# Optimization experiments

Measured on AMD Instinct MI355X. Metric: run time of the kernel, lower is better.

Reference implementation:

```python
import jax, jax.numpy as jnp
import numpy as np

N_CLASSES = 1000
N_CONCEPTS = 8
D = 512
BATCH = 4096


def setup_inputs() -> dict:
    key = jax.random.key(0)
    k1, k2 = jax.random.split(key)
    image_encodings = jax.random.normal(k1, (BATCH, D), dtype=jnp.float32)
    description_encodings = jax.random.normal(k2, (N_CLASSES, N_CONCEPTS, D), dtype=jnp.float32)
    return {"image_encodings": image_encodings, "description_encodings": description_encodings}


def reference(image_encodings, description_encodings):
    B, d = image_encodings.shape
    C, K, _ = description_encodings.shape
    # F.normalize(image_encodings, dim=-1)
    img = image_encodings / jnp.linalg.norm(image_encodings, axis=-1, keepdims=True)
    # per-class dot products, stacked over classes and flattened -> [B, C*K]
    sims = jnp.einsum("bd,ckd->bck", img, description_encodings).reshape(B, C * K)
    # descending top-K over all concept similarities (method='rank')
    _, topk_idx = jax.lax.top_k(sims, K)            # [B, K]
    concept_of_class = topk_idx // K                # class bucket of each top concept
    # log-scale rank weights: log1p(ranks)/sum, ranks = K..1
    ranks = jnp.arange(K, 0, -1, dtype=sims.dtype)
    w = jnp.log1p(ranks)
    w = w / jnp.sum(w)
    # weighted vote per class (vectorized scatter-add replaces the per-item dict loop)
    votes = jnp.zeros((B, C), dtype=sims.dtype)
    votes = votes.at[jnp.arange(B)[:, None], concept_of_class].add(w[None, :])
    # dict max over sorted unique keys == argmax with first-index tie-break
    predictions = jnp.argmax(votes, axis=1)
    confidences = jnp.take_along_axis(votes, predictions[:, None], axis=1)[:, 0]
    return predictions.astype(jnp.float32), confidences, sims
```

## Files before the change

kernel.cpp:

```cpp
#include <hip/hip_runtime.h>
#include <math.h>

#define BATCH 4096
#define D 512
#define NCLASS 1000
#define NCON 8
#define NTOT 8000
#define NPAD 8192
#define KH 1024

typedef __attribute__((ext_vector_type(8))) short bf16x8;
typedef __attribute__((ext_vector_type(4))) float f32x4;

static __device__ __forceinline__ unsigned short f2bf(float f) {
    unsigned int u = __float_as_uint(f);
    unsigned int r = (u + 0x7fffu + ((u >> 16) & 1u)) >> 16;
    return (unsigned short)r;
}
static __device__ __forceinline__ float bf2f(unsigned short h) {
    return __uint_as_float(((unsigned int)h) << 16);
}

__global__ __launch_bounds__(256) void prep_A_kernel(
    const float* __restrict__ x, unsigned short* __restrict__ Ac)
{
    const int row  = blockIdx.x * 4 + (threadIdx.x >> 6);
    const int lane = threadIdx.x & 63;
    const float4* x4 = (const float4*)(x + (size_t)row * D);
    float4 a = x4[lane];
    float4 b = x4[lane + 64];
    float s = a.x*a.x + a.y*a.y + a.z*a.z + a.w*a.w
            + b.x*b.x + b.y*b.y + b.z*b.z + b.w*b.w;
    #pragma unroll
    for (int off = 32; off; off >>= 1) s += __shfl_xor(s, off, 64);
    const float inv = 1.0f / sqrtf(s);

    float av[4] = {a.x, a.y, a.z, a.w};
    float bv[4] = {b.x, b.y, b.z, b.w};
    ushort4 ha, la, hb, lb;
    unsigned short* pha = (unsigned short*)&ha; unsigned short* pla = (unsigned short*)&la;
    unsigned short* phb = (unsigned short*)&hb; unsigned short* plb = (unsigned short*)&lb;
    #pragma unroll
    for (int c = 0; c < 4; ++c) {
        float fa = av[c] * inv;
        unsigned short h = f2bf(fa);
        pha[c] = h; pla[c] = f2bf(fa - bf2f(h));
        float fb = bv[c] * inv;
        h = f2bf(fb);
        phb[c] = h; plb[c] = f2bf(fb - bf2f(h));
    }
    unsigned short* base = Ac + (size_t)row * KH;
    const int c0 = lane * 4;
    *(ushort4*)(base + c0)        = ha;
    *(ushort4*)(base + 256 + c0)  = hb;
    *(ushort4*)(base + 512 + c0)  = la;
    *(ushort4*)(base + 768 + c0)  = lb;
}

__global__ __launch_bounds__(256) void prep_B_kernel(
    const float* __restrict__ x, unsigned short* __restrict__ Bc)
{
    const int row  = blockIdx.x * 4 + (threadIdx.x >> 6);
    const int lane = threadIdx.x & 63;
    unsigned short* base = Bc + (size_t)row * KH;
    const int c0 = lane * 4;
    if (row < NTOT) {
        const float4* x4 = (const float4*)(x + (size_t)row * D);
        float4 a = x4[lane];
        float4 b = x4[lane + 64];
        float av[4] = {a.x, a.y, a.z, a.w};
        float bv[4] = {b.x, b.y, b.z, b.w};
        ushort4 ha, la, hb, lb;
        unsigned short* pha = (unsigned short*)&ha; unsigned short* pla = (unsigned short*)&la;
        unsigned short* phb = (unsigned short*)&hb; unsigned short* plb = (unsigned short*)&lb;
        #pragma unroll
        for (int c = 0; c < 4; ++c) {
            unsigned short h = f2bf(av[c]);
            pha[c] = h; pla[c] = f2bf(av[c] - bf2f(h));
            h = f2bf(bv[c]);
            phb[c] = h; plb[c] = f2bf(bv[c] - bf2f(h));
        }
        *(ushort4*)(base + c0)        = ha;
        *(ushort4*)(base + 256 + c0)  = hb;
        *(ushort4*)(base + 512 + c0)  = la;
        *(ushort4*)(base + 768 + c0)  = lb;
    } else {
        ushort4 z = make_ushort4(0,0,0,0);
        *(ushort4*)(base + c0)        = z;
        *(ushort4*)(base + 256 + c0)  = z;
        *(ushort4*)(base + 512 + c0)  = z;
        *(ushort4*)(base + 768 + c0)  = z;
    }
}

__global__ __launch_bounds__(256) void gemm_bf16_kernel(
    const unsigned short* __restrict__ A, const unsigned short* __restrict__ B,
    float* __restrict__ C)
{
    __shared__ short sAh[128 * 32];
    __shared__ short sAl[128 * 32];
    __shared__ short sBh[128 * 32];
    __shared__ short sBl[128 * 32];

    const int tid  = threadIdx.x;
    const int w    = tid >> 6;
    const int l    = tid & 63;
    const int wm   = w >> 1;
    const int wn   = w & 1;

    const int bid = blockIdx.x;
    const int xcd = bid & 7;
    const int loc = bid >> 3;
    const int bx  = xcd * 8 + (loc & 7);
    const int by  = loc >> 3;
    const int m0  = by * 128;
    const int n0  = bx * 128;

    f32x4 acc[4][4];
    #pragma unroll
    for (int i = 0; i < 4; ++i)
        #pragma unroll
        for (int j = 0; j < 4; ++j) acc[i][j] = (f32x4){0.f, 0.f, 0.f, 0.f};

    const int srow = w * 32 + (l >> 2);
    const int scol = (l & 3) * 8;
    const unsigned short* gA0 = A + (size_t)(m0 + srow) * KH + scol;
    const unsigned short* gA1 = gA0 + (size_t)16 * KH;
    const unsigned short* gB0 = B + (size_t)(n0 + srow) * KH + scol;
    const unsigned short* gB1 = gB0 + (size_t)16 * KH;
    short* lAh0 = &sAh[(w * 32) * 32];      short* lAh1 = &sAh[(w * 32 + 16) * 32];
    short* lAl0 = &sAl[(w * 32) * 32];      short* lAl1 = &sAl[(w * 32 + 16) * 32];
    short* lBh0 = &sBh[(w * 32) * 32];      short* lBh1 = &sBh[(w * 32 + 16) * 32];
    short* lBl0 = &sBl[(w * 32) * 32];      short* lBl1 = &sBl[(w * 32 + 16) * 32];

    const int fro = (l & 15) * 32 + (l >> 4) * 8;

    for (int k0 = 0; k0 < D; k0 += 32) {
        __syncthreads();
        __builtin_amdgcn_global_load_lds((const __attribute__((address_space(1))) void*)(gA0 + k0),
            (__attribute__((address_space(3))) void*)lAh0, 16, 0, 0);
        __builtin_amdgcn_global_load_lds((const __attribute__((address_space(1))) void*)(gA1 + k0),
            (__attribute__((address_space(3))) void*)lAh1, 16, 0, 0);
        __builtin_amdgcn_global_load_lds((const __attribute__((address_space(1))) void*)(gA0 + 512 + k0),
            (__attribute__((address_space(3))) void*)lAl0, 16, 0, 0);
        __builtin_amdgcn_global_load_lds((const __attribute__((address_space(1))) void*)(gA1 + 512 + k0),
            (__attribute__((address_space(3))) void*)lAl1, 16, 0, 0);
        __builtin_amdgcn_global_load_lds((const __attribute__((address_space(1))) void*)(gB0 + k0),
            (__attribute__((address_space(3))) void*)lBh0, 16, 0, 0);
        __builtin_amdgcn_global_load_lds((const __attribute__((address_space(1))) void*)(gB1 + k0),
            (__attribute__((address_space(3))) void*)lBh1, 16, 0, 0);
        __builtin_amdgcn_global_load_lds((const __attribute__((address_space(1))) void*)(gB0 + 512 + k0),
            (__attribute__((address_space(3))) void*)lBl0, 16, 0, 0);
        __builtin_amdgcn_global_load_lds((const __attribute__((address_space(1))) void*)(gB1 + 512 + k0),
            (__attribute__((address_space(3))) void*)lBl1, 16, 0, 0);
        __syncthreads();

        bf16x8 ah[4], al[4], bh[4], bl[4];
        #pragma unroll
        for (int i = 0; i < 4; ++i) {
            ah[i] = *(const bf16x8*)&sAh[(wm * 64 + i * 16) * 32 + fro];
            al[i] = *(const bf16x8*)&sAl[(wm * 64 + i * 16) * 32 + fro];
        }
        #pragma unroll
        for (int j = 0; j < 4; ++j) {
            bh[j] = *(const bf16x8*)&sBh[(wn * 64 + j * 16) * 32 + fro];
            bl[j] = *(const bf16x8*)&sBl[(wn * 64 + j * 16) * 32 + fro];
        }

        #pragma unroll
        for (int i = 0; i < 4; ++i)
            #pragma unroll
            for (int j = 0; j < 4; ++j) {
                acc[i][j] = __builtin_amdgcn_mfma_f32_16x16x32_bf16(ah[i], bh[j], acc[i][j], 0, 0, 0);
                acc[i][j] = __builtin_amdgcn_mfma_f32_16x16x32_bf16(ah[i], bl[j], acc[i][j], 0, 0, 0);
                acc[i][j] = __builtin_amdgcn_mfma_f32_16x16x32_bf16(al[i], bh[j], acc[i][j], 0, 0, 0);
            }
    }

    #pragma unroll
    for (int i = 0; i < 4; ++i) {
        const int row = m0 + wm * 64 + i * 16 + (l >> 4) * 4;
        #pragma unroll
        for (int j = 0; j < 4; ++j) {
            const int col = n0 + wn * 64 + j * 16 + (l & 15);
            if (col < NTOT) {
                float* Cp = C + (size_t)row * NTOT + col;
                #pragma unroll
                for (int r = 0; r < 4; ++r) Cp[(size_t)r * NTOT] = acc[i][j][r];
            }
        }
    }
}

__global__ __launch_bounds__(256) void topk_vote_kernel(
    const float* __restrict__ sims, float* __restrict__ pred, float* __restrict__ conf)
{
    const int row  = blockIdx.x;
    const int tid  = threadIdx.x;
    const int wv   = tid >> 6;
    const int lane = tid & 63;
    const float4* s4 = (const float4*)(sims + (size_t)row * NTOT);

    float v[8]; int ix[8];
    #pragma unroll
    for (int i = 0; i < 8; ++i) { v[i] = -INFINITY; ix[i] = 0x7fffffff; }

    #define INS(val, idx)                                                     \
        if ((val) > v[7]) {                                                   \
            v[7] = (val); ix[7] = (idx);                                      \
            _Pragma("unroll")                                                 \
            for (int p = 7; p > 0; --p)                                       \
                if (v[p] > v[p-1]) {                                          \
                    float tv = v[p];  v[p] = v[p-1];  v[p-1] = tv;            \
                    int   ti = ix[p]; ix[p] = ix[p-1]; ix[p-1] = ti;          \
                }                                                             \
        }

    for (int p = tid; p < NTOT / 4; p += 256) {
        const float4 q = s4[p];
        const float mx = fmaxf(fmaxf(q.x, q.y), fmaxf(q.z, q.w));
        if (mx > v[7]) {
            const int j = 4 * p;
            INS(q.x, j); INS(q.y, j + 1); INS(q.z, j + 2); INS(q.w, j + 3);
        }
    }
    #undef INS

    float topv[8]; int topi[8];
    #pragma unroll
    for (int r = 0; r < 8; ++r) {
        float mv = v[0]; int mi = ix[0];
        #pragma unroll
        for (int off = 32; off; off >>= 1) {
            const float ov = __shfl_xor(mv, off, 64);
            const int   oi = __shfl_xor(mi, off, 64);
            if (ov > mv || (ov == mv && oi < mi)) { mv = ov; mi = oi; }
        }
        topv[r] = mv; topi[r] = mi;
        if (ix[0] == mi) {
            #pragma unroll
            for (int q = 0; q < 7; ++q) { v[q] = v[q+1]; ix[q] = ix[q+1]; }
            v[7] = -INFINITY; ix[7] = 0x7fffffff;
        }
    }

    __shared__ float lv[32];
    __shared__ int   li[32];
    if (lane == 0) {
        #pragma unroll
        for (int r = 0; r < 8; ++r) { lv[wv * 8 + r] = topv[r]; li[wv * 8 + r] = topi[r]; }
    }
    __syncthreads();

    if (wv == 0) {
        float mv2 = -INFINITY; int mi2 = 0x7fffffff;
        if (lane < 32) { mv2 = lv[lane]; mi2 = li[lane]; }

        float fv[8]; int fi[8];
        #pragma unroll
        for (int r = 0; r < 8; ++r) {
            float m = mv2; int mi = mi2;
            #pragma unroll
            for (int off = 32; off; off >>= 1) {
                const float ov = __shfl_xor(m, off, 64);
                const int   oi = __shfl_xor(mi, off, 64);
                if (ov > m || (ov == m && oi < mi)) { m = ov; mi = oi; }
            }
            fv[r] = m; fi[r] = mi;
            if (mi2 == mi) { mv2 = -INFINITY; mi2 = 0x7fffffff; }
        }
        (void)fv;

        float w[8]; float z = 0.f;
        #pragma unroll
        for (int r = 0; r < 8; ++r) { w[r] = log1pf((float)(8 - r)); z += w[r]; }
        #pragma unroll
        for (int r = 0; r < 8; ++r) w[r] /= z;

        float best = -1.f; int bestc = 0x7fffffff;
        #pragma unroll
        for (int r = 0; r < 8; ++r) {
            const int cr = fi[r] >> 3;
            bool dup = false;
            #pragma unroll
            for (int q = 0; q < r; ++q) dup = dup || ((fi[q] >> 3) == cr);
            float vote = w[r];
            #pragma unroll
            for (int q = r + 1; q < 8; ++q) vote += ((fi[q] >> 3) == cr) ? w[q] : 0.f;
            if (!dup && (vote > best || (vote == best && cr < bestc))) { best = vote; bestc = cr; }
        }

        if (lane == 0) { pred[row] = (float)bestc; conf[row] = best; }
    }
}

__global__ __launch_bounds__(256) void rownorm_kernel(
    const float* __restrict__ x, float* __restrict__ inv_norm)
{
    const int row  = blockIdx.x * 4 + (threadIdx.x >> 6);
    const int lane = threadIdx.x & 63;
    const float4* x4 = (const float4*)(x + (size_t)row * D);
    float4 a = x4[lane];
    float4 b = x4[lane + 64];
    float s = a.x*a.x + a.y*a.y + a.z*a.z + a.w*a.w
            + b.x*b.x + b.y*b.y + b.z*b.z + b.w*b.w;
    #pragma unroll
    for (int off = 32; off; off >>= 1) s += __shfl_xor(s, off, 64);
    if (lane == 0) inv_norm[row] = 1.0f / sqrtf(s);
}

__global__ __launch_bounds__(256) void gemm_norm_kernel(
    const float* __restrict__ A, const float* __restrict__ B,
    const float* __restrict__ invn, float* __restrict__ C)
{
    __shared__ float As[16][128];
    __shared__ float Bs[16][128];
    const int tid = threadIdx.x;
    const int tx  = tid & 15;
    const int ty  = tid >> 4;
    const int m0  = blockIdx.y * 128;
    const int n0  = blockIdx.x * 128;
    const int lr = tid >> 2;
    const int lc = (tid & 3) << 2;
    float acc[8][8];
    #pragma unroll
    for (int i = 0; i < 8; ++i)
        #pragma unroll
        for (int j = 0; j < 8; ++j) acc[i][j] = 0.f;
    const int  nr0 = n0 + lr, nr1 = n0 + lr + 64;
    const bool bv0 = nr0 < NTOT, bv1 = nr1 < NTOT;
    const float* Arow0 = A + (size_t)(m0 + lr) * D + lc;
    const float* Arow1 = Arow0 + (size_t)64 * D;
    const float* Brow0 = B + (size_t)nr0 * D + lc;
    const float* Brow1 = Brow0 + (size_t)64 * D;
    for (int k0 = 0; k0 < D; k0 += 16) {
        float4 a0 = *(const float4*)(Arow0 + k0);
        float4 a1 = *(const float4*)(Arow1 + k0);
        float4 b0 = bv0 ? *(const float4*)(Brow0 + k0) : make_float4(0.f,0.f,0.f,0.f);
        float4 b1 = bv1 ? *(const float4*)(Brow1 + k0) : make_float4(0.f,0.f,0.f,0.f);
        __syncthreads();
        As[lc+0][lr]    = a0.x; As[lc+1][lr]    = a0.y; As[lc+2][lr]    = a0.z; As[lc+3][lr]    = a0.w;
        As[lc+0][lr+64] = a1.x; As[lc+1][lr+64] = a1.y; As[lc+2][lr+64] = a1.z; As[lc+3][lr+64] = a1.w;
        Bs[lc+0][lr]    = b0.x; Bs[lc+1][lr]    = b0.y; Bs[lc+2][lr]    = b0.z; Bs[lc+3][lr]    = b0.w;
        Bs[lc+0][lr+64] = b1.x; Bs[lc+1][lr+64] = b1.y; Bs[lc+2][lr+64] = b1.z; Bs[lc+3][lr+64] = b1.w;
        __syncthreads();
        #pragma unroll
        for (int kk = 0; kk < 16; ++kk) {
            float af[8], bf[8];
            *(float4*)&af[0] = *(const float4*)&As[kk][ty*8];
            *(float4*)&af[4] = *(const float4*)&As[kk][ty*8+4];
            *(float4*)&bf[0] = *(const float4*)&Bs[kk][tx*8];
            *(float4*)&bf[4] = *(const float4*)&Bs[kk][tx*8+4];
            #pragma unroll
            for (int i = 0; i < 8; ++i)
                #pragma unroll
                for (int j = 0; j < 8; ++j)
                    acc[i][j] = fmaf(af[i], bf[j], acc[i][j]);
        }
    }
    const int col = n0 + tx * 8;
    if (col < NTOT) {
        #pragma unroll
        for (int i = 0; i < 8; ++i) {
            const int row = m0 + ty * 8 + i;
            const float s = invn[row];
            float4 o0, o1;
            o0.x = acc[i][0]*s; o0.y = acc[i][1]*s; o0.z = acc[i][2]*s; o0.w = acc[i][3]*s;
            o1.x = acc[i][4]*s; o1.y = acc[i][5]*s; o1.z = acc[i][6]*s; o1.w = acc[i][7]*s;
            float* Crow = C + (size_t)row * NTOT + col;
            *(float4*)Crow     = o0;
            *(float4*)(Crow+4) = o1;
        }
    }
}

extern "C" void kernel_launch(void* const* d_in, const int* in_sizes, int n_in,
                              void* d_out, int out_size, void* d_ws, size_t ws_size,
                              hipStream_t stream) {
    (void)in_sizes; (void)n_in; (void)out_size;
    const float* img  = (const float*)d_in[0];
    const float* desc = (const float*)d_in[1];
    float* out  = (float*)d_out;
    float* pred = out;
    float* conf = out + BATCH;
    float* sims = out + 2 * BATCH;

    const size_t szA = (size_t)BATCH * KH * sizeof(unsigned short);
    const size_t szB = (size_t)NPAD  * KH * sizeof(unsigned short);

    if (ws_size >= szA + szB) {
        unsigned short* Ac = (unsigned short*)d_ws;
        unsigned short* Bc = (unsigned short*)((char*)d_ws + szA);

        prep_A_kernel<<<BATCH / 4, 256, 0, stream>>>(img, Ac);
        prep_B_kernel<<<NPAD / 4, 256, 0, stream>>>(desc, Bc);

        gemm_bf16_kernel<<<(NPAD / 128) * (BATCH / 128), 256, 0, stream>>>(Ac, Bc, sims);
    } else {
        float* invn = (float*)d_ws;
        rownorm_kernel<<<BATCH / 4, 256, 0, stream>>>(img, invn);
        dim3 g((NTOT + 127) / 128, BATCH / 128);
        gemm_norm_kernel<<<g, 256, 0, stream>>>(img, desc, invn, sims);
    }

    topk_vote_kernel<<<BATCH, 256, 0, stream>>>(sims, pred, conf);
}
```

Before: 287.4 us.

## Merge prep kernels and split top-k scan across two blocks per row

Fuses the two bf16 hi/lo split prep kernels into one launch covering image and description rows. Replaces the one-block-per-row top-k/vote kernel with a two-block-per-row scan that writes 8 candidates per half to workspace, followed by a small merge-and-vote kernel with one wave per row. The aim is to cut a launch and double the parallelism of the top-k pass. The cost is an extra launch plus candidate traffic through workspace, and the workspace requirement grows.

```diff
diff --git a/kernel.cpp b/kernel.cpp
--- a/kernel.cpp
+++ b/kernel.cpp
@@ -21,53 +21,25 @@
     return __uint_as_float(((unsigned int)h) << 16);
 }
 
-__global__ __launch_bounds__(256) void prep_A_kernel(
-    const float* __restrict__ x, unsigned short* __restrict__ Ac)
-{
-    const int row  = blockIdx.x * 4 + (threadIdx.x >> 6);
+__global__ __launch_bounds__(256) void prep_kernel(
+    const float* __restrict__ img, const float* __restrict__ desc,
+    unsigned short* __restrict__ Ac, unsigned short* __restrict__ Bc)
+{
+    const int gr   = blockIdx.x * 4 + (threadIdx.x >> 6);
     const int lane = threadIdx.x & 63;
-    const float4* x4 = (const float4*)(x + (size_t)row * D);
-    float4 a = x4[lane];
-    float4 b = x4[lane + 64];
-    float s = a.x*a.x + a.y*a.y + a.z*a.z + a.w*a.w
-            + b.x*b.x + b.y*b.y + b.z*b.z + b.w*b.w;
-    #pragma unroll
-    for (int off = 32; off; off >>= 1) s += __shfl_xor(s, off, 64);
-    const float inv = 1.0f / sqrtf(s);
-
-    float av[4] = {a.x, a.y, a.z, a.w};
-    float bv[4] = {b.x, b.y, b.z, b.w};
-    ushort4 ha, la, hb, lb;
-    unsigned short* pha = (unsigned short*)&ha; unsigned short* pla = (unsigned short*)&la;
-    unsigned short* phb = (unsigned short*)&hb; unsigned short* plb = (unsigned short*)&lb;
-    #pragma unroll
-    for (int c = 0; c < 4; ++c) {
-        float fa = av[c] * inv;
-        unsigned short h = f2bf(fa);
-        pha[c] = h; pla[c] = f2bf(fa - bf2f(h));
-        float fb = bv[c] * inv;
-        h = f2bf(fb);
-        phb[c] = h; plb[c] = f2bf(fb - bf2f(h));
-    }
-    unsigned short* base = Ac + (size_t)row * KH;
-    const int c0 = lane * 4;
-    *(ushort4*)(base + c0)        = ha;
-    *(ushort4*)(base + 256 + c0)  = hb;
-    *(ushort4*)(base + 512 + c0)  = la;
-    *(ushort4*)(base + 768 + c0)  = lb;
-}
-
-__global__ __launch_bounds__(256) void prep_B_kernel(
-    const float* __restrict__ x, unsigned short* __restrict__ Bc)
-{
-    const int row  = blockIdx.x * 4 + (threadIdx.x >> 6);
-    const int lane = threadIdx.x & 63;
-    unsigned short* base = Bc + (size_t)row * KH;
-    const int c0 = lane * 4;
-    if (row < NTOT) {
-        const float4* x4 = (const float4*)(x + (size_t)row * D);
+    const int c0   = lane * 4;
+
+    if (gr < BATCH) {
+        const int row = gr;
+        const float4* x4 = (const float4*)(img + (size_t)row * D);
         float4 a = x4[lane];
         float4 b = x4[lane + 64];
+        float s = a.x*a.x + a.y*a.y + a.z*a.z + a.w*a.w
+                + b.x*b.x + b.y*b.y + b.z*b.z + b.w*b.w;
+        #pragma unroll
+        for (int off = 32; off; off >>= 1) s += __shfl_xor(s, off, 64);
+        const float inv = 1.0f / sqrtf(s);
+
         float av[4] = {a.x, a.y, a.z, a.w};
         float bv[4] = {b.x, b.y, b.z, b.w};
         ushort4 ha, la, hb, lb;
@@ -75,21 +47,48 @@
         unsigned short* phb = (unsigned short*)&hb; unsigned short* plb = (unsigned short*)&lb;
         #pragma unroll
         for (int c = 0; c < 4; ++c) {
-            unsigned short h = f2bf(av[c]);
-            pha[c] = h; pla[c] = f2bf(av[c] - bf2f(h));
-            h = f2bf(bv[c]);
-            phb[c] = h; plb[c] = f2bf(bv[c] - bf2f(h));
-        }
+            float fa = av[c] * inv;
+            unsigned short h = f2bf(fa);
+            pha[c] = h; pla[c] = f2bf(fa - bf2f(h));
+            float fb = bv[c] * inv;
+            h = f2bf(fb);
+            phb[c] = h; plb[c] = f2bf(fb - bf2f(h));
+        }
+        unsigned short* base = Ac + (size_t)row * KH;
         *(ushort4*)(base + c0)        = ha;
         *(ushort4*)(base + 256 + c0)  = hb;
         *(ushort4*)(base + 512 + c0)  = la;
         *(ushort4*)(base + 768 + c0)  = lb;
     } else {
-        ushort4 z = make_ushort4(0,0,0,0);
-        *(ushort4*)(base + c0)        = z;
-        *(ushort4*)(base + 256 + c0)  = z;
-        *(ushort4*)(base + 512 + c0)  = z;
-        *(ushort4*)(base + 768 + c0)  = z;
+        const int row = gr - BATCH;
+        unsigned short* base = Bc + (size_t)row * KH;
+        if (row < NTOT) {
+            const float4* x4 = (const float4*)(desc + (size_t)row * D);
+            float4 a = x4[lane];
+            float4 b = x4[lane + 64];
+            float av[4] = {a.x, a.y, a.z, a.w};
+            float bv[4] = {b.x, b.y, b.z, b.w};
+            ushort4 ha, la, hb, lb;
+            unsigned short* pha = (unsigned short*)&ha; unsigned short* pla = (unsigned short*)&la;
+            unsigned short* phb = (unsigned short*)&hb; unsigned short* plb = (unsigned short*)&lb;
+            #pragma unroll
+            for (int c = 0; c < 4; ++c) {
+                unsigned short h = f2bf(av[c]);
+                pha[c] = h; pla[c] = f2bf(av[c] - bf2f(h));
+                h = f2bf(bv[c]);
+                phb[c] = h; plb[c] = f2bf(bv[c] - bf2f(h));
+            }
+            *(ushort4*)(base + c0)        = ha;
+            *(ushort4*)(base + 256 + c0)  = hb;
+            *(ushort4*)(base + 512 + c0)  = la;
+            *(ushort4*)(base + 768 + c0)  = lb;
+        } else {
+            ushort4 z = make_ushort4(0,0,0,0);
+            *(ushort4*)(base + c0)        = z;
+            *(ushort4*)(base + 256 + c0)  = z;
+            *(ushort4*)(base + 512 + c0)  = z;
+            *(ushort4*)(base + 768 + c0)  = z;
+        }
     }
 }
 
@@ -192,14 +191,16 @@
     }
 }
 
-__global__ __launch_bounds__(256) void topk_vote_kernel(
-    const float* __restrict__ sims, float* __restrict__ pred, float* __restrict__ conf)
-{
-    const int row  = blockIdx.x;
+__global__ __launch_bounds__(256) void topk_scan_kernel(
+    const float* __restrict__ sims, float* __restrict__ candV, int* __restrict__ candI)
+{
+    const int row  = blockIdx.x >> 1;
+    const int half = blockIdx.x & 1;
     const int tid  = threadIdx.x;
     const int wv   = tid >> 6;
     const int lane = tid & 63;
-    const float4* s4 = (const float4*)(sims + (size_t)row * NTOT);
+    const float4* s4   = (const float4*)(sims + (size_t)row * NTOT);
+    const int     base = half * 1000;
 
     float v[8]; int ix[8];
     #pragma unroll
@@ -216,12 +217,16 @@
                 }                                                             \
         }
 
-    for (int p = tid; p < NTOT / 4; p += 256) {
-        const float4 q = s4[p];
-        const float mx = fmaxf(fmaxf(q.x, q.y), fmaxf(q.z, q.w));
-        if (mx > v[7]) {
-            const int j = 4 * p;
-            INS(q.x, j); INS(q.y, j + 1); INS(q.z, j + 2); INS(q.w, j + 3);
+    #pragma unroll
+    for (int i = 0; i < 4; ++i) {
+        const int p4 = base + tid + i * 256;
+        if (p4 < base + 1000) {
+            const float4 q = s4[p4];
+            const float mx = fmaxf(fmaxf(q.x, q.y), fmaxf(q.z, q.w));
+            if (mx > v[7]) {
+                const int j = 4 * p4;
+                INS(q.x, j); INS(q.y, j + 1); INS(q.z, j + 2); INS(q.w, j + 3);
+            }
         }
     }
     #undef INS
@@ -253,8 +258,8 @@
     __syncthreads();
 
     if (wv == 0) {
-        float mv2 = -INFINITY; int mi2 = 0x7fffffff;
-        if (lane < 32) { mv2 = lv[lane]; mi2 = li[lane]; }
+        float mv2 = (lane < 32) ? lv[lane] : -INFINITY;
+        int   mi2 = (lane < 32) ? li[lane] : 0x7fffffff;
 
         float fv[8]; int fi[8];
         #pragma unroll
@@ -269,29 +274,60 @@
             fv[r] = m; fi[r] = mi;
             if (mi2 == mi) { mv2 = -INFINITY; mi2 = 0x7fffffff; }
         }
-        (void)fv;
-
-        float w[8]; float z = 0.f;
-        #pragma unroll
-        for (int r = 0; r < 8; ++r) { w[r] = log1pf((float)(8 - r)); z += w[r]; }
-        #pragma unroll
-        for (int r = 0; r < 8; ++r) w[r] /= z;
-
-        float best = -1.f; int bestc = 0x7fffffff;
-        #pragma unroll
-        for (int r = 0; r < 8; ++r) {
-            const int cr = fi[r] >> 3;
-            bool dup = false;
-            #pragma unroll
-            for (int q = 0; q < r; ++q) dup = dup || ((fi[q] >> 3) == cr);
-            float vote = w[r];
-            #pragma unroll
-            for (int q = r + 1; q < 8; ++q) vote += ((fi[q] >> 3) == cr) ? w[q] : 0.f;
-            if (!dup && (vote > best || (vote == best && cr < bestc))) { best = vote; bestc = cr; }
-        }
-
-        if (lane == 0) { pred[row] = (float)bestc; conf[row] = best; }
-    }
+
+        if (lane == 0) {
+            float* cv = candV + (size_t)row * 16 + half * 8;
+            int*   ci = candI + (size_t)row * 16 + half * 8;
+            #pragma unroll
+            for (int r = 0; r < 8; ++r) { cv[r] = fv[r]; ci[r] = fi[r]; }
+        }
+    }
+}
+
+__global__ __launch_bounds__(256) void merge_vote_kernel(
+    const float* __restrict__ candV, const int* __restrict__ candI,
+    float* __restrict__ pred, float* __restrict__ conf)
+{
+    const int row  = blockIdx.x * 4 + (threadIdx.x >> 6);
+    const int lane = threadIdx.x & 63;
+
+    float mv = (lane < 16) ? candV[(size_t)row * 16 + lane] : -INFINITY;
+    int   mi = (lane < 16) ? candI[(size_t)row * 16 + lane] : 0x7fffffff;
+
+    int fi[8];
+    #pragma unroll
+    for (int r = 0; r < 8; ++r) {
+        float m = mv; int i = mi;
+        #pragma unroll
+        for (int off = 32; off; off >>= 1) {
+            const float ov = __shfl_xor(m, off, 64);
+            const int   oi = __shfl_xor(i, off, 64);
+            if (ov > m || (ov == m && oi < i)) { m = ov; i = oi; }
+        }
+        fi[r] = i;
+        if (mi == i) { mv = -INFINITY; mi = 0x7fffffff; }
+    }
+
+    float w[8]; float z = 0.f;
+    #pragma unroll
+    for (int r = 0; r < 8; ++r) { w[r] = log1pf((float)(8 - r)); z += w[r]; }
+    #pragma unroll
+    for (int r = 0; r < 8; ++r) w[r] /= z;
+
+    float best = -1.f; int bestc = 0x7fffffff;
+    #pragma unroll
+    for (int r = 0; r < 8; ++r) {
+        const int cr = fi[r] >> 3;
+        bool dup = false;
+        #pragma unroll
+        for (int q = 0; q < r; ++q) dup = dup || ((fi[q] >> 3) == cr);
+        float vote = w[r];
+        #pragma unroll
+        for (int q = r + 1; q < 8; ++q) vote += ((fi[q] >> 3) == cr) ? w[q] : 0.f;
+        if (!dup && (vote > best || (vote == best && cr < bestc))) { best = vote; bestc = cr; }
+    }
+
+    if (lane == 0) { pred[row] = (float)bestc; conf[row] = best; }
 }
 
 __global__ __launch_bounds__(256) void rownorm_kernel(
@@ -374,6 +410,108 @@
     }
 }
 
+__global__ __launch_bounds__(256) void topk_vote_kernel(
+    const float* __restrict__ sims, float* __restrict__ pred, float* __restrict__ conf)
+{
+    const int row  = blockIdx.x;
+    const int tid  = threadIdx.x;
+    const int wv   = tid >> 6;
+    const int lane = tid & 63;
+    const float4* s4 = (const float4*)(sims + (size_t)row * NTOT);
+
+    float v[8]; int ix[8];
+    #pragma unroll
+    for (int i = 0; i < 8; ++i) { v[i] = -INFINITY; ix[i] = 0x7fffffff; }
+
+    #define INS(val, idx)                                                     \
+        if ((val) > v[7]) {                                                   \
+            v[7] = (val); ix[7] = (idx);                                      \
+            _Pragma("unroll")                                                 \
+            for (int p = 7; p > 0; --p)                                       \
+                if (v[p] > v[p-1]) {                                          \
+                    float tv = v[p];  v[p] = v[p-1];  v[p-1] = tv;            \
+                    int   ti = ix[p]; ix[p] = ix[p-1]; ix[p-1] = ti;          \
+                }                                                             \
+        }
+
+    for (int p = tid; p < NTOT / 4; p += 256) {
+        const float4 q = s4[p];
+        const float mx = fmaxf(fmaxf(q.x, q.y), fmaxf(q.z, q.w));
+        if (mx > v[7]) {
+            const int j = 4 * p;
+            INS(q.x, j); INS(q.y, j + 1); INS(q.z, j + 2); INS(q.w, j + 3);
+        }
+    }
+    #undef INS
+
+    float topv[8]; int topi[8];
+    #pragma unroll
+    for (int r = 0; r < 8; ++r) {
+        float mv = v[0]; int mi = ix[0];
+        #pragma unroll
+        for (int off = 32; off; off >>= 1) {
+            const float ov = __shfl_xor(mv, off, 64);
+            const int   oi = __shfl_xor(mi, off, 64);
+            if (ov > mv || (ov == mv && oi < mi)) { mv = ov; mi = oi; }
+        }
+        topv[r] = mv; topi[r] = mi;
+        if (ix[0] == mi) {
+            #pragma unroll
+            for (int q = 0; q < 7; ++q) { v[q] = v[q+1]; ix[q] = ix[q+1]; }
+            v[7] = -INFINITY; ix[7] = 0x7fffffff;
+        }
+    }
+
+    __shared__ float lv[32];
+    __shared__ int   li[32];
+    if (lane == 0) {
+        #pragma unroll
+        for (int r = 0; r < 8; ++r) { lv[wv * 8 + r] = topv[r]; li[wv * 8 + r] = topi[r]; }
+    }
+    __syncthreads();
+
+    if (wv == 0) {
+        float mv2 = (lane < 32) ? lv[lane] : -INFINITY;
+        int   mi2 = (lane < 32) ? li[lane] : 0x7fffffff;
+
+        float fv[8]; int fi[8];
+        #pragma unroll
+        for (int r = 0; r < 8; ++r) {
+            float m = mv2; int mi = mi2;
+            #pragma unroll
+            for (int off = 32; off; off >>= 1) {
+                const float ov = __shfl_xor(m, off, 64);
+                const int   oi = __shfl_xor(mi, off, 64);
+                if (ov > m || (ov == m && oi < mi)) { m = ov; mi = oi; }
+            }
+            fv[r] = m; fi[r] = mi;
+            if (mi2 == mi) { mv2 = -INFINITY; mi2 = 0x7fffffff; }
+        }
+        (void)fv;
+
+        float w[8]; float z = 0.f;
+        #pragma unroll
+        for (int r = 0; r < 8; ++r) { w[r] = log1pf((float)(8 - r)); z += w[r]; }
+        #pragma unroll
+        for (int r = 0; r < 8; ++r) w[r] /= z;
+
+        float best = -1.f; int bestc = 0x7fffffff;
+        #pragma unroll
+        for (int r = 0; r < 8; ++r) {
+            const int cr = fi[r] >> 3;
+            bool dup = false;
+            #pragma unroll
+            for (int q = 0; q < r; ++q) dup = dup || ((fi[q] >> 3) == cr);
+            float vote = w[r];
+            #pragma unroll
+            for (int q = r + 1; q < 8; ++q) vote += ((fi[q] >> 3) == cr) ? w[q] : 0.f;
+            if (!dup && (vote > best || (vote == best && cr < bestc))) { best = vote; bestc = cr; }
+        }
+
+        if (lane == 0) { pred[row] = (float)bestc; conf[row] = best; }
+    }
+}
+
 extern "C" void kernel_launch(void* const* d_in, const int* in_sizes, int n_in,
                               void* d_out, int out_size, void* d_ws, size_t ws_size,
                               hipStream_t stream) {
@@ -387,21 +525,24 @@
 
     const size_t szA = (size_t)BATCH * KH * sizeof(unsigned short);
     const size_t szB = (size_t)NPAD  * KH * sizeof(unsigned short);
-
-    if (ws_size >= szA + szB) {
+    const size_t szCv = (size_t)BATCH * 16 * sizeof(float);
+    const size_t szCi = (size_t)BATCH * 16 * sizeof(int);
+
+    if (ws_size >= szA + szB + szCv + szCi) {
         unsigned short* Ac = (unsigned short*)d_ws;
         unsigned short* Bc = (unsigned short*)((char*)d_ws + szA);
-
-        prep_A_kernel<<<BATCH / 4, 256, 0, stream>>>(img, Ac);
-        prep_B_kernel<<<NPAD / 4, 256, 0, stream>>>(desc, Bc);
-
+        float* candV = (float*)((char*)d_ws + szA + szB);
+        int*   candI = (int*)((char*)d_ws + szA + szB + szCv);
+
+        prep_kernel<<<(BATCH + NPAD) / 4, 256, 0, stream>>>(img, desc, Ac, Bc);
         gemm_bf16_kernel<<<(NPAD / 128) * (BATCH / 128), 256, 0, stream>>>(Ac, Bc, sims);
+        topk_scan_kernel<<<BATCH * 2, 256, 0, stream>>>(sims, candV, candI);
+        merge_vote_kernel<<<BATCH / 4, 256, 0, stream>>>(candV, candI, pred, conf);
     } else {
         float* invn = (float*)d_ws;
         rownorm_kernel<<<BATCH / 4, 256, 0, stream>>>(img, invn);
         dim3 g((NTOT + 127) / 128, BATCH / 128);
         gemm_norm_kernel<<<g, 256, 0, stream>>>(img, desc, invn, sims);
-    }
-
-    topk_vote_kernel<<<BATCH, 256, 0, stream>>>(sims, pred, conf);
-}
+        topk_vote_kernel<<<BATCH, 256, 0, stream>>>(sims, pred, conf);
+    }
+}
```

Result: slower. 301.7 us (+5.0%).
